# Optimization experiments

Measured on AMD Instinct MI355X. Metric: run time of the kernel, lower is better.

The kernel has to match this reference:

```python
import jax, jax.numpy as jnp
import numpy as np

N, E, D, H = 100000, 400000, 128, 128  # nodes, edges, feat dim, mlp hidden


def _ln(x, g, b, eps=1e-5):
    m = jnp.mean(x, axis=-1, keepdims=True)
    v = jnp.mean((x - m) ** 2, axis=-1, keepdims=True)
    return (x - m) * jax.lax.rsqrt(v + eps) * g + b


def _mlp(x, w0, b0, w1, b1, w2, b2):
    # Linear->ReLU->Linear->ReLU->Linear (last act = Identity)
    h = jax.nn.relu(x @ w0 + b0)
    h = jax.nn.relu(h @ w1 + b1)
    return h @ w2 + b2


def setup_inputs() -> dict:
    key = jax.random.key(0)
    ks = jax.random.split(key, 16)
    node_x = jax.random.normal(ks[0], (N, D), dtype=jnp.float32)
    edge_attr = jax.random.normal(ks[1], (E, D), dtype=jnp.float32)
    edge_index = jax.random.randint(ks[2], (2, E), 0, N, dtype=jnp.int32)

    def lin(k, fin, fout):
        kw, kb = jax.random.split(k)
        s = 1.0 / np.sqrt(fin)
        w = jax.random.uniform(kw, (fin, fout), jnp.float32, -s, s)
        b = jax.random.uniform(kb, (fout,), jnp.float32, -s, s)
        return w, b

    # message MLP: (3D) -> H -> H -> D, then LayerNorm(D)
    msg_w0, msg_b0 = lin(ks[3], 3 * D, H)
    msg_w1, msg_b1 = lin(ks[4], H, H)
    msg_w2, msg_b2 = lin(ks[5], H, D)
    # top-level update MLP: (D + D) -> H -> H -> D, then LayerNorm(D)
    upd_w0, upd_b0 = lin(ks[6], 2 * D, H)
    upd_w1, upd_b1 = lin(ks[7], H, H)
    upd_w2, upd_b2 = lin(ks[8], H, D)
    return {
        "node_x": node_x, "edge_attr": edge_attr, "edge_index": edge_index,
        "msg_w0": msg_w0, "msg_b0": msg_b0, "msg_w1": msg_w1, "msg_b1": msg_b1,
        "msg_w2": msg_w2, "msg_b2": msg_b2,
        "msg_g": jnp.ones((D,), jnp.float32), "msg_beta": jnp.zeros((D,), jnp.float32),
        "upd_w0": upd_w0, "upd_b0": upd_b0, "upd_w1": upd_w1, "upd_b1": upd_b1,
        "upd_w2": upd_w2, "upd_b2": upd_b2,
        "upd_g": jnp.ones((D,), jnp.float32), "upd_beta": jnp.zeros((D,), jnp.float32),
    }


def reference(node_x, edge_attr, edge_index,
              msg_w0, msg_b0, msg_w1, msg_b1, msg_w2, msg_b2, msg_g, msg_beta,
              upd_w0, upd_b0, upd_w1, upd_b1, upd_w2, upd_b2, upd_g, upd_beta):
    src, dst = edge_index[0], edge_index[1]
    # PyG default flow source_to_target: x_j = x[src], x_i = x[dst]
    x_i = node_x[dst]                       # [E, D]
    x_j = node_x[src]                       # [E, D]
    concat = jnp.concatenate([x_i, x_j, edge_attr], axis=1)  # [E, 3D]
    msg = _ln(_mlp(concat, msg_w0, msg_b0, msg_w1, msg_b1, msg_w2, msg_b2), msg_g, msg_beta)
    new_edge = edge_attr + msg              # edge_attr[:] += msg in original
    # scatter-add messages onto target nodes
    agg = jax.ops.segment_sum(new_edge, dst, num_segments=N)  # [N, D]
    concat2 = jnp.concatenate([node_x, agg], axis=1)          # [N, 2D]
    upd = _ln(_mlp(concat2, upd_w0, upd_b0, upd_w1, upd_b1, upd_w2, upd_b2), upd_g, upd_beta)
    return node_x + upd
```

## Files before the change

kernel.cpp:

```cpp
#include <hip/hip_runtime.h>

typedef __attribute__((ext_vector_type(4))) float f32x4;
typedef __attribute__((ext_vector_type(8))) __bf16 bf16x8;

constexpr int FD = 128;

__device__ __forceinline__ uint4 pack8(const float* v) {
  union { __bf16 h[8]; uint4 u; } cv;
#pragma unroll
  for (int q = 0; q < 8; ++q) cv.h[q] = (__bf16)v[q];
  return cv.u;
}
__device__ __forceinline__ unsigned int pack2(float a, float b) {
  union { __bf16 h[2]; unsigned int u; } cv;
  cv.h[0] = (__bf16)a; cv.h[1] = (__bf16)b;
  return cv.u;
}

__global__ void cvt_bf16(const float* __restrict__ x, unsigned short* __restrict__ o, int n8) {
  int i = blockIdx.x * 256 + threadIdx.x;
  if (i >= n8) return;
  const float* p = x + (size_t)i * 8;
  float v[8];
#pragma unroll
  for (int q = 0; q < 8; ++q) v[q] = p[q];
  *(uint4*)(o + (size_t)i * 8) = pack8(v);
}

__global__ void pack_weights(const float* __restrict__ mw0, const float* __restrict__ mw1,
                             const float* __restrict__ mw2, const float* __restrict__ uw0,
                             const float* __restrict__ uw1, const float* __restrict__ uw2,
                             unsigned short* __restrict__ wp) {
  int tid = blockIdx.x * 256 + threadIdx.x;
  const float* src; int base, K;
  if      (tid < 49152)  { src = mw0; base = 0;      K = 384; }
  else if (tid < 65536)  { src = mw1; base = 49152;  K = 128; }
  else if (tid < 81920)  { src = mw2; base = 65536;  K = 128; }
  else if (tid < 114688) { src = uw0; base = 81920;  K = 256; }
  else if (tid < 131072) { src = uw1; base = 114688; K = 128; }
  else                   { src = uw2; base = 131072; K = 128; }
  int i = tid - base;
  int k = i >> 7, n = i & 127;
  int KS = K >> 5;
  int dst = base + (((n >> 4) * KS + (k >> 5)) * 64 + ((k >> 3) & 3) * 16 + (n & 15)) * 8 + (k & 7);
  union { __bf16 h; unsigned short s; } cv; cv.h = (__bf16)src[i];
  wp[dst] = cv.s;
}

template<int KSTEPS>
__device__ __forceinline__ void mfma_gB(const unsigned short* __restrict__ wsrc,
                                        const unsigned short* sAsrc, int strideA,
                                        f32x4* acc, int w, int lane, int g16, int ln) {
#pragma unroll
  for (int ks = 0; ks < KSTEPS; ++ks) {
    bf16x8 b = *(const bf16x8*)(wsrc + (size_t)((w * KSTEPS + ks) * 64 + lane) * 8);
#pragma unroll
    for (int m = 0; m < 4; ++m) {
      bf16x8 a = *(const bf16x8*)&sAsrc[(m * 16 + ln) * strideA + ks * 32 + g16 * 8];
      acc[m] = __builtin_amdgcn_mfma_f32_16x16x32_bf16(a, b, acc[m], 0, 0, 0);
    }
  }
}

template<int KSTEPS>
__device__ __forceinline__ void mfma_rB(const bf16x8* B,
                                        const unsigned short* sAsrc, int strideA,
                                        f32x4* acc, int g16, int ln) {
#pragma unroll
  for (int ks = 0; ks < KSTEPS; ++ks) {
#pragma unroll
    for (int m = 0; m < 4; ++m) {
      bf16x8 a = *(const bf16x8*)&sAsrc[(m * 16 + ln) * strideA + ks * 32 + g16 * 8];
      acc[m] = __builtin_amdgcn_mfma_f32_16x16x32_bf16(a, B[ks], acc[m], 0, 0, 0);
    }
  }
}

template<bool RELU>
__device__ __forceinline__ void store_tile(unsigned short* sDst, int stride,
                                           const f32x4* acc, float bias, int col, int g16) {
#pragma unroll
  for (int m = 0; m < 4; ++m)
#pragma unroll
    for (int ri = 0; ri < 4; ++ri) {
      float v = acc[m][ri] + bias;
      if (RELU) v = fmaxf(v, 0.f);
      union { __bf16 h; unsigned short s; } cv; cv.h = (__bf16)v;
      sDst[(m * 16 + g16 * 4 + ri) * stride + col] = cv.s;
    }
}

__global__ __launch_bounds__(512, 6)
void in_edge_kernel(const float* __restrict__ node_x, const unsigned short* __restrict__ nxbf,
                    const float* __restrict__ edge_attr,
                    const int* __restrict__ eidx, const unsigned short* __restrict__ wp,
                    const float* __restrict__ b0p, const float* __restrict__ b1p,
                    const float* __restrict__ b2p, const float* __restrict__ gp,
                    const float* __restrict__ bep,
                    unsigned short* __restrict__ msg, int* __restrict__ head,
                    int* __restrict__ nxt, float* __restrict__ agg,
                    int use_sort, int E) {
  __shared__ unsigned short sA[64 * 392];
  __shared__ int sSrc[64], sDst[64];
  __shared__ float sG[128], sB[128];

  const int t = threadIdx.x;
  const int e0 = blockIdx.x * 64;
  const int lane = t & 63, w = t >> 6;
  const int ln = lane & 15, g16 = lane >> 4;
  const int col = w * 16 + ln;

  bf16x8 B1r[4], B2r[4];
#pragma unroll
  for (int ks = 0; ks < 4; ++ks)
    B1r[ks] = *(const bf16x8*)(wp + 49152 + (size_t)((w * 4 + ks) * 64 + lane) * 8);
#pragma unroll
  for (int ks = 0; ks < 4; ++ks)
    B2r[ks] = *(const bf16x8*)(wp + 65536 + (size_t)((w * 4 + ks) * 64 + lane) * 8);

  if (t < 64) {
    sSrc[t] = (e0 + t < E) ? eidx[e0 + t] : 0;
  } else if (t < 128) {
    int r = t - 64;
    int e = e0 + r;
    int d = (e < E) ? eidx[E + e] : 0;
    sDst[r] = d;
    if (use_sort && e < E) nxt[e] = atomicExch(&head[d], e);
  } else if (t < 256) {
    sG[t - 128] = gp[t - 128];
  } else if (t < 384) {
    sB[t - 256] = bep[t - 256];
  }
  __syncthreads();

  if (nxbf) {
#pragma unroll
    for (int it = 0; it < 2; ++it) {
      int f = t + it * 512;
      int row = f >> 4, j = f & 15;
      uint4 v = {0, 0, 0, 0}, u = {0, 0, 0, 0};
      if (e0 + row < E) {
        v = *(const uint4*)(nxbf + (size_t)sDst[row] * FD + j * 8);
        u = *(const uint4*)(nxbf + (size_t)sSrc[row] * FD + j * 8);
      }
      *(uint4*)&sA[row * 392 + j * 8] = v;
      *(uint4*)&sA[row * 392 + 128 + j * 8] = u;
    }
  } else {
#pragma unroll
    for (int it = 0; it < 16; ++it) {
      const int type = it >> 3;
      int row = ((it & 7) << 3) + w;
      float2 v = {0.f, 0.f};
      if (e0 + row < E) {
        const float* sp = (type == 0) ? node_x + (size_t)sDst[row] * FD
                                      : node_x + (size_t)sSrc[row] * FD;
        v = *(const float2*)(sp + lane * 2);
      }
      *(unsigned int*)&sA[row * 392 + type * 128 + lane * 2] = pack2(v.x, v.y);
    }
  }
#pragma unroll
  for (int it = 0; it < 8; ++it) {
    int row = it * 8 + w;
    float2 v = {0.f, 0.f};
    if (e0 + row < E) v = *(const float2*)(edge_attr + (size_t)(e0 + row) * FD + lane * 2);
    *(unsigned int*)&sA[row * 392 + 256 + lane * 2] = pack2(v.x, v.y);
  }
  __syncthreads();

  const float b0v = b0p[col], b1v = b1p[col], b2v = b2p[col];

  f32x4 acc[4];
#pragma unroll
  for (int m = 0; m < 4; ++m) acc[m] = (f32x4){0.f, 0.f, 0.f, 0.f};

  mfma_gB<12>(wp, sA, 392, acc, w, lane, g16, ln);
  __syncthreads();
  store_tile<true>(sA, 392, acc, b0v, col, g16);
  __syncthreads();

#pragma unroll
  for (int m = 0; m < 4; ++m) acc[m] = (f32x4){0.f, 0.f, 0.f, 0.f};
  mfma_rB<4>(B1r, sA, 392, acc, g16, ln);
  store_tile<true>(sA + 128, 392, acc, b1v, col, g16);
  __syncthreads();

#pragma unroll
  for (int m = 0; m < 4; ++m) acc[m] = (f32x4){0.f, 0.f, 0.f, 0.f};
  mfma_rB<4>(B2r, sA + 128, 392, acc, g16, ln);
  store_tile<false>(sA, 392, acc, b2v, col, g16);
  __syncthreads();

  {
    int row = t >> 3, j = t & 7;
    bf16x8 v0 = *(const bf16x8*)&sA[row * 392 + j * 16];
    bf16x8 v1 = *(const bf16x8*)&sA[row * 392 + j * 16 + 8];
    float s1 = 0.f, s2 = 0.f;
#pragma unroll
    for (int q = 0; q < 8; ++q) {
      float a = (float)v0[q], b = (float)v1[q];
      s1 += a + b; s2 += a * a + b * b;
    }
#pragma unroll
    for (int m = 1; m < 8; m <<= 1) {
      s1 += __shfl_xor(s1, m, 64);
      s2 += __shfl_xor(s2, m, 64);
    }
    float mean = s1 * (1.f / 128.f);
    float var  = s2 * (1.f / 128.f) - mean * mean;
    float rstd = rsqrtf(fmaxf(var, 0.f) + 1e-5f);

    int e = e0 + row;
    if (e < E) {
      bf16x8 ea0 = *(const bf16x8*)&sA[row * 392 + 256 + j * 16];
      bf16x8 ea1 = *(const bf16x8*)&sA[row * 392 + 256 + j * 16 + 8];
      float val[16];
#pragma unroll
      for (int q = 0; q < 8; ++q) {
        val[q]     = ((float)v0[q] - mean) * rstd * sG[j * 16 + q]     + sB[j * 16 + q]     + (float)ea0[q];
        val[8 + q] = ((float)v1[q] - mean) * rstd * sG[j * 16 + 8 + q] + sB[j * 16 + 8 + q] + (float)ea1[q];
      }
      if (use_sort) {
        uint4* dst = (uint4*)(msg + (size_t)e * FD + j * 16);
        dst[0] = pack8(val);
        dst[1] = pack8(val + 8);
      } else {
        float* ap = agg + (size_t)sDst[row] * FD + j * 16;
#pragma unroll
        for (int q = 0; q < 16; ++q) atomicAdd(ap + q, val[q]);
      }
    }
  }
}

__global__ __launch_bounds__(512, 8)
void in_node_kernel(const float* __restrict__ node_x, const unsigned short* __restrict__ nxbf,
                    const unsigned short* __restrict__ msg, const int* __restrict__ head,
                    const int* __restrict__ nxt, const float* __restrict__ agg,
                    const unsigned short* __restrict__ wp,
                    const float* __restrict__ b0p, const float* __restrict__ b1p,
                    const float* __restrict__ b2p, const float* __restrict__ gp,
                    const float* __restrict__ bep, float* __restrict__ out,
                    int use_sort, int N) {
  __shared__ unsigned short sA[64 * 264];
  __shared__ float sG[128], sB[128];

  const int t = threadIdx.x;
  const int r0 = blockIdx.x * 64;
  const int lane = t & 63, w = t >> 6;
  const int ln = lane & 15, g16 = lane >> 4;
  const int col = w * 16 + ln;

  bf16x8 B1r[4], B2r[4];
#pragma unroll
  for (int ks = 0; ks < 4; ++ks)
    B1r[ks] = *(const bf16x8*)(wp + 114688 + (size_t)((w * 4 + ks) * 64 + lane) * 8);
#pragma unroll
  for (int ks = 0; ks < 4; ++ks)
    B2r[ks] = *(const bf16x8*)(wp + 131072 + (size_t)((w * 4 + ks) * 64 + lane) * 8);

  if (t < 128)      sG[t] = gp[t];
  else if (t < 256) sB[t - 128] = bep[t - 128];

  if (nxbf) {
#pragma unroll
    for (int it = 0; it < 2; ++it) {
      int f = t + it * 512;
      int row = f >> 4, j = f & 15;
      int r = r0 + row;
      uint4 v = {0, 0, 0, 0};
      if (r < N) v = *(const uint4*)(nxbf + (size_t)r * FD + j * 8);
      *(uint4*)&sA[row * 264 + j * 8] = v;
    }
  } else {
#pragma unroll
    for (int it = 0; it < 8; ++it) {
      int row = (it << 3) + w;
      int r = r0 + row;
      float2 v = {0.f, 0.f};
      if (r < N) v = *(const float2*)(node_x + (size_t)r * FD + lane * 2);
      *(unsigned int*)&sA[row * 264 + lane * 2] = pack2(v.x, v.y);
    }
  }

  {
    int row = t >> 3, j = t & 7;
    int node = r0 + row;
    float a[16];
#pragma unroll
    for (int q = 0; q < 16; ++q) a[q] = 0.f;
    if (node < N) {
      if (use_sort) {
        int e = head[node];
        while (e >= 0) {
          int ne = nxt[e];
          bf16x8 m0 = *(const bf16x8*)(msg + (size_t)e * FD + j * 16);
          bf16x8 m1 = *(const bf16x8*)(msg + (size_t)e * FD + j * 16 + 8);
#pragma unroll
          for (int q = 0; q < 8; ++q) { a[q] += (float)m0[q]; a[8 + q] += (float)m1[q]; }
          e = ne;
        }
      } else {
        const float* ap = agg + (size_t)node * FD + j * 16;
#pragma unroll
        for (int q4 = 0; q4 < 4; ++q4) {
          f32x4 u = *(const f32x4*)(ap + q4 * 4);
#pragma unroll
          for (int q = 0; q < 4; ++q) a[q4 * 4 + q] = u[q];
        }
      }
    }
    uint4* dst = (uint4*)&sA[row * 264 + 128 + j * 16];
    dst[0] = pack8(a);
    dst[1] = pack8(a + 8);
  }
  __syncthreads();

  const float b0v = b0p[col], b1v = b1p[col], b2v = b2p[col];

  f32x4 acc[4];
#pragma unroll
  for (int m = 0; m < 4; ++m) acc[m] = (f32x4){0.f, 0.f, 0.f, 0.f};

  mfma_gB<8>(wp + 81920, sA, 264, acc, w, lane, g16, ln);
  __syncthreads();
  store_tile<true>(sA, 264, acc, b0v, col, g16);
  __syncthreads();

#pragma unroll
  for (int m = 0; m < 4; ++m) acc[m] = (f32x4){0.f, 0.f, 0.f, 0.f};
  mfma_rB<4>(B1r, sA, 264, acc, g16, ln);
  store_tile<true>(sA + 128, 264, acc, b1v, col, g16);
  __syncthreads();

#pragma unroll
  for (int m = 0; m < 4; ++m) acc[m] = (f32x4){0.f, 0.f, 0.f, 0.f};
  mfma_rB<4>(B2r, sA + 128, 264, acc, g16, ln);
  store_tile<false>(sA, 264, acc, b2v, col, g16);
  __syncthreads();

  {
    int row = t >> 3, j = t & 7;
    bf16x8 v0 = *(const bf16x8*)&sA[row * 264 + j * 16];
    bf16x8 v1 = *(const bf16x8*)&sA[row * 264 + j * 16 + 8];
    float s1 = 0.f, s2 = 0.f;
#pragma unroll
    for (int q = 0; q < 8; ++q) {
      float a = (float)v0[q], b = (float)v1[q];
      s1 += a + b; s2 += a * a + b * b;
    }
#pragma unroll
    for (int m = 1; m < 8; m <<= 1) {
      s1 += __shfl_xor(s1, m, 64);
      s2 += __shfl_xor(s2, m, 64);
    }
    float mean = s1 * (1.f / 128.f);
    float var  = s2 * (1.f / 128.f) - mean * mean;
    float rstd = rsqrtf(fmaxf(var, 0.f) + 1e-5f);

    int node = r0 + row;
    if (node < N) {
      float o[16];
#pragma unroll
      for (int q = 0; q < 8; ++q) {
        o[q]     = ((float)v0[q] - mean) * rstd * sG[j * 16 + q]     + sB[j * 16 + q];
        o[8 + q] = ((float)v1[q] - mean) * rstd * sG[j * 16 + 8 + q] + sB[j * 16 + 8 + q];
      }
      const float* xr = node_x + (size_t)node * FD + j * 16;
      float* orow = out + (size_t)node * FD + j * 16;
#pragma unroll
      for (int q4 = 0; q4 < 4; ++q4) {
        f32x4 x = *(const f32x4*)(xr + q4 * 4);
        f32x4 wv;
#pragma unroll
        for (int q = 0; q < 4; ++q) wv[q] = o[q4 * 4 + q] + x[q];
        *(f32x4*)(orow + q4 * 4) = wv;
      }
    }
  }
}

extern "C" void kernel_launch(void* const* d_in, const int* in_sizes, int n_in,
                              void* d_out, int out_size, void* d_ws, size_t ws_size,
                              hipStream_t stream) {
  const float* node_x    = (const float*)d_in[0];
  const float* edge_attr = (const float*)d_in[1];
  const int*   eidx      = (const int*)d_in[2];
  const int N = in_sizes[0] / FD;
  const int E = in_sizes[1] / FD;

  char* ws = (char*)d_ws;
  auto aln = [](size_t x) { return (x + 255) & ~(size_t)255; };
  const size_t wpB   = aln(294912);
  const size_t nxbfB = aln((size_t)N * FD * 2);
  const size_t headB = aln((size_t)N * 4);
  const size_t nxtB  = aln((size_t)E * 4);
  const size_t msgB  = (size_t)E * FD * 2;

  unsigned short* wp = (unsigned short*)ws;
  unsigned short* nxbf = nullptr;
  int* head = nullptr; int* nxt = nullptr;
  unsigned short* msg = nullptr; float* agg = nullptr;
  int use_sort = 0;

  if (ws_size >= wpB + nxbfB + headB + nxtB + msgB) {
    use_sort = 1;
    nxbf = (unsigned short*)(ws + wpB);
    head = (int*)(ws + wpB + nxbfB);
    nxt  = (int*)(ws + wpB + nxbfB + headB);
    msg  = (unsigned short*)(ws + wpB + nxbfB + headB + nxtB);
  } else if (ws_size >= wpB + headB + nxtB + msgB) {
    use_sort = 1;
    head = (int*)(ws + wpB);
    nxt  = (int*)(ws + wpB + headB);
    msg  = (unsigned short*)(ws + wpB + headB + nxtB);
  } else {
    agg = (float*)(ws + wpB);
  }

  if (use_sort) (void)hipMemsetAsync(head, 0xFF, (size_t)N * 4, stream);
  else          (void)hipMemsetAsync(agg, 0, (size_t)N * FD * sizeof(float), stream);

  pack_weights<<<576, 256, 0, stream>>>(
      (const float*)d_in[3], (const float*)d_in[5], (const float*)d_in[7],
      (const float*)d_in[11], (const float*)d_in[13], (const float*)d_in[15], wp);
  if (nxbf) cvt_bf16<<<(N * FD / 8 + 255) / 256, 256, 0, stream>>>(node_x, nxbf, N * FD / 8);
  in_edge_kernel<<<(E + 63) / 64, 512, 0, stream>>>(
      node_x, nxbf, edge_attr, eidx, wp,
      (const float*)d_in[4], (const float*)d_in[6], (const float*)d_in[8],
      (const float*)d_in[9], (const float*)d_in[10],
      msg, head, nxt, agg, use_sort, E);
  in_node_kernel<<<(N + 63) / 64, 512, 0, stream>>>(
      node_x, nxbf, msg, head, nxt, agg, wp,
      (const float*)d_in[12], (const float*)d_in[14], (const float*)d_in[16],
      (const float*)d_in[17], (const float*)d_in[18], (float*)d_out, use_sort, N);
}
```

Baseline: 278.1 us.

## Store LDS activations in MFMA fragment-packed layout and prefetch weights in a ring

Replaces the padded row-major shared-memory tile with a layout packed by MFMA fragment, so A-operand reads become contiguous 16-byte loads at fixed offsets and bank conflicts drop. Layer-0 weights are now loaded as a rolling register ring (6 or 4 steps ahead) instead of per-step global loads, and later-layer weights are loaded after the first GEMM to lower peak register pressure. The shared buffer shrinks a little. In exchange, every load, store and LayerNorm read needs more complex index arithmetic, which adds correctness risk.

```diff
diff --git a/kernel.cpp b/kernel.cpp
--- a/kernel.cpp
+++ b/kernel.cpp
@@ -47,38 +47,9 @@
   wp[dst] = cv.s;
 }
 
-template<int KSTEPS>
-__device__ __forceinline__ void mfma_gB(const unsigned short* __restrict__ wsrc,
-                                        const unsigned short* sAsrc, int strideA,
-                                        f32x4* acc, int w, int lane, int g16, int ln) {
-#pragma unroll
-  for (int ks = 0; ks < KSTEPS; ++ks) {
-    bf16x8 b = *(const bf16x8*)(wsrc + (size_t)((w * KSTEPS + ks) * 64 + lane) * 8);
-#pragma unroll
-    for (int m = 0; m < 4; ++m) {
-      bf16x8 a = *(const bf16x8*)&sAsrc[(m * 16 + ln) * strideA + ks * 32 + g16 * 8];
-      acc[m] = __builtin_amdgcn_mfma_f32_16x16x32_bf16(a, b, acc[m], 0, 0, 0);
-    }
-  }
-}
-
-template<int KSTEPS>
-__device__ __forceinline__ void mfma_rB(const bf16x8* B,
-                                        const unsigned short* sAsrc, int strideA,
-                                        f32x4* acc, int g16, int ln) {
-#pragma unroll
-  for (int ks = 0; ks < KSTEPS; ++ks) {
-#pragma unroll
-    for (int m = 0; m < 4; ++m) {
-      bf16x8 a = *(const bf16x8*)&sAsrc[(m * 16 + ln) * strideA + ks * 32 + g16 * 8];
-      acc[m] = __builtin_amdgcn_mfma_f32_16x16x32_bf16(a, B[ks], acc[m], 0, 0, 0);
-    }
-  }
-}
 
 template<bool RELU>
-__device__ __forceinline__ void store_tile(unsigned short* sDst, int stride,
-                                           const f32x4* acc, float bias, int col, int g16) {
+__device__ __forceinline__ void store_frag(unsigned short* sDst, const f32x4* acc, float bias) {
 #pragma unroll
   for (int m = 0; m < 4; ++m)
 #pragma unroll
@@ -86,7 +57,7 @@
       float v = acc[m][ri] + bias;
       if (RELU) v = fmaxf(v, 0.f);
       union { __bf16 h; unsigned short s; } cv; cv.h = (__bf16)v;
-      sDst[(m * 16 + g16 * 4 + ri) * stride + col] = cv.s;
+      sDst[m * 512 + ri * 32] = cv.s;
     }
 }
 
@@ -100,7 +71,7 @@
                     unsigned short* __restrict__ msg, int* __restrict__ head,
                     int* __restrict__ nxt, float* __restrict__ agg,
                     int use_sort, int E) {
-  __shared__ unsigned short sA[64 * 392];
+  __shared__ unsigned short sBuf[3072 * 8];
   __shared__ int sSrc[64], sDst[64];
   __shared__ float sG[128], sB[128];
 
@@ -109,14 +80,18 @@
   const int lane = t & 63, w = t >> 6;
   const int ln = lane & 15, g16 = lane >> 4;
   const int col = w * 16 + ln;
-
-  bf16x8 B1r[4], B2r[4];
+  const int rdoff = ln * 32 + g16 * 8;
+  const int stoff = (w >> 1) * 2048 + g16 * 128
+                  + (((2 * w) + (ln >> 3)) & 3) * 8 + (ln & 7);
+
+  bf16x8 b0[6];
+#pragma unroll
+  for (int ks = 0; ks < 6; ++ks)
+    b0[ks] = *(const bf16x8*)(wp + (size_t)((w * 12 + ks) * 64 + lane) * 8);
+  bf16x8 B1r[4];
 #pragma unroll
   for (int ks = 0; ks < 4; ++ks)
     B1r[ks] = *(const bf16x8*)(wp + 49152 + (size_t)((w * 4 + ks) * 64 + lane) * 8);
-#pragma unroll
-  for (int ks = 0; ks < 4; ++ks)
-    B2r[ks] = *(const bf16x8*)(wp + 65536 + (size_t)((w * 4 + ks) * 64 + lane) * 8);
 
   if (t < 64) {
     sSrc[t] = (e0 + t < E) ? eidx[e0 + t] : 0;
@@ -143,8 +118,9 @@
         v = *(const uint4*)(nxbf + (size_t)sDst[row] * FD + j * 8);
         u = *(const uint4*)(nxbf + (size_t)sSrc[row] * FD + j * 8);
       }
-      *(uint4*)&sA[row * 392 + j * 8] = v;
-      *(uint4*)&sA[row * 392 + 128 + j * 8] = u;
+      int c = (((j >> 2) * 4 + (row >> 4)) * 64 + (row & 15) * 4 + (j & 3)) * 8;
+      *(uint4*)&sBuf[c] = v;
+      *(uint4*)&sBuf[c + 8192] = u;
     }
   } else {
 #pragma unroll
@@ -157,7 +133,9 @@
                                       : node_x + (size_t)sSrc[row] * FD;
         v = *(const float2*)(sp + lane * 2);
       }
-      *(unsigned int*)&sA[row * 392 + type * 128 + lane * 2] = pack2(v.x, v.y);
+      int c = (((type * 4 + (lane >> 4)) * 4 + (row >> 4)) * 64
+               + (row & 15) * 4 + ((lane >> 2) & 3)) * 8 + (lane & 3) * 2;
+      *(unsigned int*)&sBuf[c] = pack2(v.x, v.y);
     }
   }
 #pragma unroll
@@ -165,7 +143,9 @@
     int row = it * 8 + w;
     float2 v = {0.f, 0.f};
     if (e0 + row < E) v = *(const float2*)(edge_attr + (size_t)(e0 + row) * FD + lane * 2);
-    *(unsigned int*)&sA[row * 392 + 256 + lane * 2] = pack2(v.x, v.y);
+    int c = 16384 + (((lane >> 4) * 4 + (row >> 4)) * 64
+                     + (row & 15) * 4 + ((lane >> 2) & 3)) * 8 + (lane & 3) * 2;
+    *(unsigned int*)&sBuf[c] = pack2(v.x, v.y);
   }
   __syncthreads();
 
@@ -175,27 +155,55 @@
 #pragma unroll
   for (int m = 0; m < 4; ++m) acc[m] = (f32x4){0.f, 0.f, 0.f, 0.f};
 
-  mfma_gB<12>(wp, sA, 392, acc, w, lane, g16, ln);
-  __syncthreads();
-  store_tile<true>(sA, 392, acc, b0v, col, g16);
-  __syncthreads();
-
-#pragma unroll
-  for (int m = 0; m < 4; ++m) acc[m] = (f32x4){0.f, 0.f, 0.f, 0.f};
-  mfma_rB<4>(B1r, sA, 392, acc, g16, ln);
-  store_tile<true>(sA + 128, 392, acc, b1v, col, g16);
-  __syncthreads();
-
-#pragma unroll
-  for (int m = 0; m < 4; ++m) acc[m] = (f32x4){0.f, 0.f, 0.f, 0.f};
-  mfma_rB<4>(B2r, sA + 128, 392, acc, g16, ln);
-  store_tile<false>(sA, 392, acc, b2v, col, g16);
+#pragma unroll
+  for (int ks = 0; ks < 12; ++ks) {
+    bf16x8 bb = b0[ks % 6];
+    if (ks + 6 < 12)
+      b0[ks % 6] = *(const bf16x8*)(wp + (size_t)((w * 12 + ks + 6) * 64 + lane) * 8);
+#pragma unroll
+    for (int m = 0; m < 4; ++m) {
+      bf16x8 a = *(const bf16x8*)&sBuf[(ks * 4 + m) * 512 + rdoff];
+      acc[m] = __builtin_amdgcn_mfma_f32_16x16x32_bf16(a, bb, acc[m], 0, 0, 0);
+    }
+  }
+  bf16x8 B2r[4];
+#pragma unroll
+  for (int ks = 0; ks < 4; ++ks)
+    B2r[ks] = *(const bf16x8*)(wp + 65536 + (size_t)((w * 4 + ks) * 64 + lane) * 8);
+
+  __syncthreads();
+  store_frag<true>(sBuf + stoff, acc, b0v);
+  __syncthreads();
+
+#pragma unroll
+  for (int m = 0; m < 4; ++m) acc[m] = (f32x4){0.f, 0.f, 0.f, 0.f};
+#pragma unroll
+  for (int ks = 0; ks < 4; ++ks)
+#pragma unroll
+    for (int m = 0; m < 4; ++m) {
+      bf16x8 a = *(const bf16x8*)&sBuf[(ks * 4 + m) * 512 + rdoff];
+      acc[m] = __builtin_amdgcn_mfma_f32_16x16x32_bf16(a, B1r[ks], acc[m], 0, 0, 0);
+    }
+  store_frag<true>(sBuf + 8192 + stoff, acc, b1v);
+  __syncthreads();
+
+#pragma unroll
+  for (int m = 0; m < 4; ++m) acc[m] = (f32x4){0.f, 0.f, 0.f, 0.f};
+#pragma unroll
+  for (int ks = 0; ks < 4; ++ks)
+#pragma unroll
+    for (int m = 0; m < 4; ++m) {
+      bf16x8 a = *(const bf16x8*)&sBuf[8192 + (ks * 4 + m) * 512 + rdoff];
+      acc[m] = __builtin_amdgcn_mfma_f32_16x16x32_bf16(a, B2r[ks], acc[m], 0, 0, 0);
+    }
+  store_frag<false>(sBuf + stoff, acc, b2v);
   __syncthreads();
 
   {
     int row = t >> 3, j = t & 7;
-    bf16x8 v0 = *(const bf16x8*)&sA[row * 392 + j * 16];
-    bf16x8 v1 = *(const bf16x8*)&sA[row * 392 + j * 16 + 8];
+    int a0 = (((j >> 1) * 4 + (row >> 4)) * 64 + (row & 15) * 4 + 2 * (j & 1)) * 8;
+    bf16x8 v0 = *(const bf16x8*)&sBuf[a0];
+    bf16x8 v1 = *(const bf16x8*)&sBuf[a0 + 8];
     float s1 = 0.f, s2 = 0.f;
 #pragma unroll
     for (int q = 0; q < 8; ++q) {
@@ -213,8 +221,8 @@
 
     int e = e0 + row;
     if (e < E) {
-      bf16x8 ea0 = *(const bf16x8*)&sA[row * 392 + 256 + j * 16];
-      bf16x8 ea1 = *(const bf16x8*)&sA[row * 392 + 256 + j * 16 + 8];
+      bf16x8 ea0 = *(const bf16x8*)&sBuf[a0 + 16384];
+      bf16x8 ea1 = *(const bf16x8*)&sBuf[a0 + 16384 + 8];
       float val[16];
 #pragma unroll
       for (int q = 0; q < 8; ++q) {
@@ -243,7 +251,7 @@
                     const float* __restrict__ b2p, const float* __restrict__ gp,
                     const float* __restrict__ bep, float* __restrict__ out,
                     int use_sort, int N) {
-  __shared__ unsigned short sA[64 * 264];
+  __shared__ unsigned short sBuf[2048 * 8];
   __shared__ float sG[128], sB[128];
 
   const int t = threadIdx.x;
@@ -251,14 +259,14 @@
   const int lane = t & 63, w = t >> 6;
   const int ln = lane & 15, g16 = lane >> 4;
   const int col = w * 16 + ln;
-
-  bf16x8 B1r[4], B2r[4];
-#pragma unroll
-  for (int ks = 0; ks < 4; ++ks)
-    B1r[ks] = *(const bf16x8*)(wp + 114688 + (size_t)((w * 4 + ks) * 64 + lane) * 8);
-#pragma unroll
-  for (int ks = 0; ks < 4; ++ks)
-    B2r[ks] = *(const bf16x8*)(wp + 131072 + (size_t)((w * 4 + ks) * 64 + lane) * 8);
+  const int rdoff = ln * 32 + g16 * 8;
+  const int stoff = (w >> 1) * 2048 + g16 * 128
+                  + (((2 * w) + (ln >> 3)) & 3) * 8 + (ln & 7);
+
+  bf16x8 b0[4];
+#pragma unroll
+  for (int ks = 0; ks < 4; ++ks)
+    b0[ks] = *(const bf16x8*)(wp + 81920 + (size_t)((w * 8 + ks) * 64 + lane) * 8);
 
   if (t < 128)      sG[t] = gp[t];
   else if (t < 256) sB[t - 128] = bep[t - 128];
@@ -271,7 +279,8 @@
       int r = r0 + row;
       uint4 v = {0, 0, 0, 0};
       if (r < N) v = *(const uint4*)(nxbf + (size_t)r * FD + j * 8);
-      *(uint4*)&sA[row * 264 + j * 8] = v;
+      int c = (((j >> 2) * 4 + (row >> 4)) * 64 + (row & 15) * 4 + (j & 3)) * 8;
+      *(uint4*)&sBuf[c] = v;
     }
   } else {
 #pragma unroll
@@ -280,7 +289,9 @@
       int r = r0 + row;
       float2 v = {0.f, 0.f};
       if (r < N) v = *(const float2*)(node_x + (size_t)r * FD + lane * 2);
-      *(unsigned int*)&sA[row * 264 + lane * 2] = pack2(v.x, v.y);
+      int c = (((lane >> 4) * 4 + (row >> 4)) * 64
+               + (row & 15) * 4 + ((lane >> 2) & 3)) * 8 + (lane & 3) * 2;
+      *(unsigned int*)&sBuf[c] = pack2(v.x, v.y);
     }
   }
 
@@ -311,9 +322,9 @@
         }
       }
     }
-    uint4* dst = (uint4*)&sA[row * 264 + 128 + j * 16];
-    dst[0] = pack8(a);
-    dst[1] = pack8(a + 8);
+    int c = 8192 + (((j >> 1) * 4 + (row >> 4)) * 64 + (row & 15) * 4 + 2 * (j & 1)) * 8;
+    *(uint4*)&sBuf[c] = pack8(a);
+    *(uint4*)&sBuf[c + 8] = pack8(a + 8);
   }
   __syncthreads();
 
@@ -323,27 +334,59 @@
 #pragma unroll
   for (int m = 0; m < 4; ++m) acc[m] = (f32x4){0.f, 0.f, 0.f, 0.f};
 
-  mfma_gB<8>(wp + 81920, sA, 264, acc, w, lane, g16, ln);
-  __syncthreads();
-  store_tile<true>(sA, 264, acc, b0v, col, g16);
-  __syncthreads();
-
-#pragma unroll
-  for (int m = 0; m < 4; ++m) acc[m] = (f32x4){0.f, 0.f, 0.f, 0.f};
-  mfma_rB<4>(B1r, sA, 264, acc, g16, ln);
-  store_tile<true>(sA + 128, 264, acc, b1v, col, g16);
-  __syncthreads();
-
-#pragma unroll
-  for (int m = 0; m < 4; ++m) acc[m] = (f32x4){0.f, 0.f, 0.f, 0.f};
-  mfma_rB<4>(B2r, sA + 128, 264, acc, g16, ln);
-  store_tile<false>(sA, 264, acc, b2v, col, g16);
+#pragma unroll
+  for (int ks = 0; ks < 8; ++ks) {
+    bf16x8 bb = b0[ks % 4];
+    if (ks + 4 < 8)
+      b0[ks % 4] = *(const bf16x8*)(wp + 81920 + (size_t)((w * 8 + ks + 4) * 64 + lane) * 8);
+#pragma unroll
+    for (int m = 0; m < 4; ++m) {
+      bf16x8 a = *(const bf16x8*)&sBuf[(ks * 4 + m) * 512 + rdoff];
+      acc[m] = __builtin_amdgcn_mfma_f32_16x16x32_bf16(a, bb, acc[m], 0, 0, 0);
+    }
+  }
+  bf16x8 B1r[4];
+#pragma unroll
+  for (int ks = 0; ks < 4; ++ks)
+    B1r[ks] = *(const bf16x8*)(wp + 114688 + (size_t)((w * 4 + ks) * 64 + lane) * 8);
+
+  __syncthreads();
+  store_frag<true>(sBuf + stoff, acc, b0v);
+  __syncthreads();
+
+#pragma unroll
+  for (int m = 0; m < 4; ++m) acc[m] = (f32x4){0.f, 0.f, 0.f, 0.f};
+#pragma unroll
+  for (int ks = 0; ks < 4; ++ks)
+#pragma unroll
+    for (int m = 0; m < 4; ++m) {
+      bf16x8 a = *(const bf16x8*)&sBuf[(ks * 4 + m) * 512 + rdoff];
+      acc[m] = __builtin_amdgcn_mfma_f32_16x16x32_bf16(a, B1r[ks], acc[m], 0, 0, 0);
+    }
+  bf16x8 B2r[4];
+#pragma unroll
+  for (int ks = 0; ks < 4; ++ks)
+    B2r[ks] = *(const bf16x8*)(wp + 131072 + (size_t)((w * 4 + ks) * 64 + lane) * 8);
+  store_frag<true>(sBuf + 8192 + stoff, acc, b1v);
+  __syncthreads();
+
+#pragma unroll
+  for (int m = 0; m < 4; ++m) acc[m] = (f32x4){0.f, 0.f, 0.f, 0.f};
+#pragma unroll
+  for (int ks = 0; ks < 4; ++ks)
+#pragma unroll
+    for (int m = 0; m < 4; ++m) {
+      bf16x8 a = *(const bf16x8*)&sBuf[8192 + (ks * 4 + m) * 512 + rdoff];
+      acc[m] = __builtin_amdgcn_mfma_f32_16x16x32_bf16(a, B2r[ks], acc[m], 0, 0, 0);
+    }
+  store_frag<false>(sBuf + stoff, acc, b2v);
   __syncthreads();
 
   {
     int row = t >> 3, j = t & 7;
-    bf16x8 v0 = *(const bf16x8*)&sA[row * 264 + j * 16];
-    bf16x8 v1 = *(const bf16x8*)&sA[row * 264 + j * 16 + 8];
+    int a0 = (((j >> 1) * 4 + (row >> 4)) * 64 + (row & 15) * 4 + 2 * (j & 1)) * 8;
+    bf16x8 v0 = *(const bf16x8*)&sBuf[a0];
+    bf16x8 v1 = *(const bf16x8*)&sBuf[a0 + 8];
     float s1 = 0.f, s2 = 0.f;
 #pragma unroll
     for (int q = 0; q < 8; ++q) {
```

Measured after the change: 239.4 us. 13.9% less time.
